# Kernel optimization log

Hardware: AMD Instinct MI355X
Metric: run time of the kernel (lower is better)

The kernel has to match this reference:

```python
import jax, jax.numpy as jnp
import numpy as np

B = 1024          # batch
H = 512           # hidden_dim
T = 256           # seq_len
CD = 2            # coord_dim
LAT = 64 + 64 + 128  # total latent dim


def setup_inputs() -> dict:
    key = jax.random.key(0)
    ks = jax.random.split(key, 20)
    s = 0.05  # weight init scale
    rn = lambda k, shp: (jax.random.normal(k, shp, dtype=jnp.float32) * s)
    return {
        "z_primitive": jax.random.normal(ks[0], (B, 64), dtype=jnp.float32),
        "z_skill": jax.random.normal(ks[1], (B, 64), dtype=jnp.float32),
        "z_style": jax.random.normal(ks[2], (B, 128), dtype=jnp.float32),
        "W_proj": rn(ks[3], (2 * H, LAT)),
        "b_proj": jnp.zeros((2 * H,), jnp.float32),
        "Wih1": rn(ks[4], (4 * H, CD)),
        "Whh1": rn(ks[5], (4 * H, H)),
        "bih1": jnp.zeros((4 * H,), jnp.float32),
        "bhh1": jnp.zeros((4 * H,), jnp.float32),
        "Wih2": rn(ks[6], (4 * H, H)),
        "Whh2": rn(ks[7], (4 * H, H)),
        "bih2": jnp.zeros((4 * H,), jnp.float32),
        "bhh2": jnp.zeros((4 * H,), jnp.float32),
        "Wo1": rn(ks[8], (H // 2, H)),
        "bo1": jnp.zeros((H // 2,), jnp.float32),
        "Wo2": rn(ks[9], (CD, H // 2)),
        "bo2": jnp.zeros((CD,), jnp.float32),
    }


def _lstm_cell(x, h, c, Wih, Whh, bih, bhh):
    # PyTorch gate order: i, f, g, o
    gates = x @ Wih.T + h @ Whh.T + (bih + bhh)
    i, f, g, o = jnp.split(gates, 4, axis=1)
    c_new = jax.nn.sigmoid(f) * c + jax.nn.sigmoid(i) * jnp.tanh(g)
    h_new = jax.nn.sigmoid(o) * jnp.tanh(c_new)
    return h_new, c_new


def reference(z_primitive, z_skill, z_style, W_proj, b_proj,
              Wih1, Whh1, bih1, bhh1, Wih2, Whh2, bih2, bhh2,
              Wo1, bo1, Wo2, bo2):
    z = jnp.concatenate([z_primitive, z_skill, z_style], axis=1)  # [B, LAT]
    init = z @ W_proj.T + b_proj                                  # [B, 2H]
    h0 = init[:, :H]
    c0 = init[:, H:]
    x0 = jnp.zeros((z.shape[0], CD), init.dtype)

    def step(carry, _):
        x, h1, c1, h2, c2 = carry
        h1, c1 = _lstm_cell(x, h1, c1, Wih1, Whh1, bih1, bhh1)
        h2, c2 = _lstm_cell(h1, h2, c2, Wih2, Whh2, bih2, bhh2)
        # output MLP (Dropout inactive in eval)
        y = jax.nn.relu(h2 @ Wo1.T + bo1) @ Wo2.T + bo2  # [B, CD]
        return (y, h1, c1, h2, c2), y

    # h0/c0 repeated across both LSTM layers (repeat(2,1,1) in torch)
    _, ys = jax.lax.scan(step, (x0, h0, c0, h0, c0), None, length=T)
    return jnp.transpose(ys, (1, 0, 2))  # [B, T, CD]
```

## Files before the change

kernel.cpp:

```cpp
#include <hip/hip_runtime.h>
#include <math.h>

#define NB 1024
#define NH 512
#define NT 256
#define NCD 2

typedef unsigned short u16;
typedef __bf16 bf16x8 __attribute__((ext_vector_type(8)));
typedef float  f32x4  __attribute__((ext_vector_type(4)));

#define MFMA_BF16 __builtin_amdgcn_mfma_f32_16x16x32_bf16

__device__ __forceinline__ float sigf(float x) { return 1.0f / (1.0f + expf(-x)); }
__device__ __forceinline__ float b2f(u16 u) {
    union { unsigned i; float f; } v; v.i = ((unsigned)u) << 16; return v.f;
}
__device__ __forceinline__ u16 f2b(float f) {
    union { float f; unsigned i; } v; v.f = f;
    unsigned r = v.i + 0x7fffu + ((v.i >> 16) & 1u);
    return (u16)(r >> 16);
}

__device__ __forceinline__ void async_cp16(const void* gptr, void* lptr) {
    __builtin_amdgcn_global_load_lds(
        (const __attribute__((address_space(1))) unsigned int*)gptr,
        (__attribute__((address_space(3))) unsigned int*)lptr,
        16, 0, 0);
}

__global__ __launch_bounds__(256) void convert3(
    const float* __restrict__ a, const float* __restrict__ b,
    const float* __restrict__ c,
    u16* __restrict__ oa, u16* __restrict__ ob, u16* __restrict__ oc)
{
    const int i = blockIdx.x * 256 + threadIdx.x;
    oa[i] = f2b(a[i]); ob[i] = f2b(b[i]); oc[i] = f2b(c[i]);
}

__global__ __launch_bounds__(256) void convw1(
    const float* __restrict__ a, u16* __restrict__ o)
{
    const int i = blockIdx.x * 256 + threadIdx.x;
    o[i] = f2b(a[i]);
}

__global__ __launch_bounds__(256) void bsum_k(
    const float* __restrict__ bi1, const float* __restrict__ bh1,
    const float* __restrict__ bi2, const float* __restrict__ bh2,
    float* __restrict__ o1, float* __restrict__ o2)
{
    const int i = blockIdx.x * 256 + threadIdx.x;
    o1[i] = bi1[i] + bh1[i];
    o2[i] = bi2[i] + bh2[i];
}

__global__ __launch_bounds__(256) void init_kernel(
    const float* __restrict__ zp, const float* __restrict__ zs,
    const float* __restrict__ zst, const float* __restrict__ Wp,
    const float* __restrict__ bp,
    u16* __restrict__ h1, float* __restrict__ c1,
    u16* __restrict__ h2, float* __restrict__ c2)
{
    __shared__ float z[4][256];
    const int tid = threadIdx.x;
    const int b0  = blockIdx.x * 4;
    for (int i = tid; i < 4 * 256; i += 256) {
        const int bb = i >> 8, k = i & 255;
        float v;
        if (k < 64)       v = zp [(b0 + bb) * 64  + k];
        else if (k < 128) v = zs [(b0 + bb) * 64  + (k - 64)];
        else              v = zst[(b0 + bb) * 128 + (k - 128)];
        z[bb][k] = v;
    }
    __syncthreads();
    for (int rt = 0; rt < 4; ++rt) {
        const int r = rt * 256 + tid;
        const float bias = bp[r];
        float a0 = bias, a1 = bias, a2 = bias, a3 = bias;
        for (int k = 0; k < 256; ++k) {
            const float w = Wp[r * 256 + k];
            a0 += z[0][k] * w; a1 += z[1][k] * w;
            a2 += z[2][k] * w; a3 += z[3][k] * w;
        }
        const float acc[4] = {a0, a1, a2, a3};
        for (int bb = 0; bb < 4; ++bb) {
            const int b = b0 + bb;
            if (r < NH) {
                h1[b * NH + r] = f2b(acc[bb]);
                h2[b * NH + r] = f2b(acc[bb]);
            } else {
                c1[b * NH + r - NH] = acc[bb];
                c2[b * NH + r - NH] = acc[bb];
            }
        }
    }
}

__global__ __launch_bounds__(512, 4) void fused_out_lstm1(
    const u16* __restrict__ h2prev,
    const u16* __restrict__ A0,
    const u16* __restrict__ W0,
    const float* __restrict__ bsum,
    const float* __restrict__ Wx,
    const u16* __restrict__ W1b,
    const float* __restrict__ bo1, const float* __restrict__ Wo2,
    const float* __restrict__ bo2, float* __restrict__ outp,
    float* __restrict__ c, u16* __restrict__ hnext,
    const int t, const int do_lstm)
{
    __shared__ __align__(16) char smem[61440];
    float* eg  = (float*)smem;
    float* red = (float*)(smem + 36864);

    const int tid  = threadIdx.x;
    const int lane = tid & 63;
    const int wv   = tid >> 6;
    const int g    = wv & 3;
    const int mh   = wv >> 2;
    const int l15  = lane & 15;
    const int q    = lane >> 4;
    const int bx   = blockIdx.x;
    const int ut   = (bx & 7) * 2 + ((bx >> 3) & 1);
    const int grp  = bx >> 4;
    const int b0   = grp * 32;
    const int u0   = ut * 32;

    int goffW0, goffW1, goffA = 0, goffO[4];
    {
        const int c0 = (wv * 2) * 64 + lane;
        const int w0r = c0 >> 3;
        goffW0 = ((w0r >> 5) * NH + u0 + (w0r & 31)) * NH + (((c0 & 7) ^ (w0r & 7)) * 8);
        const int c1i = (wv * 2 + 1) * 64 + lane;
        const int w1r = c1i >> 3;
        goffW1 = ((w1r >> 5) * NH + u0 + (w1r & 31)) * NH + (((c1i & 7) ^ (w1r & 7)) * 8);
        if (wv < 4) {
            const int ca = wv * 64 + lane;
            const int ar = ca >> 3;
            goffA = (b0 + ar) * NH + (((ca & 7) ^ (ar & 7)) * 8);
        }
#pragma unroll
        for (int i = 0; i < 4; ++i) {
            const int cidx = (wv * 4 + i) * 64 + lane;
            const int row  = cidx >> 3;
            const int kc   = (cidx & 7) ^ (row & 7);
            goffO[i] = row * NH + kc * 8;
        }
    }

    float r_x[4] = {0.f, 0.f, 0.f, 0.f};

    if (h2prev) {
        f32x4 acc_o[2][2];
#pragma unroll
        for (int mi = 0; mi < 2; ++mi)
#pragma unroll
            for (int ni = 0; ni < 2; ++ni)
                acc_o[mi][ni] = (f32x4){0.f, 0.f, 0.f, 0.f};

        for (int kk = 0; kk < 8; ++kk) {
            __syncthreads();
            const int k0 = kk * 64;
#pragma unroll
            for (int i = 0; i < 4; ++i)
                async_cp16((const void*)(W1b + goffO[i] + k0),
                           (void*)(smem + ((wv * 4 + i) << 10)));
            if (wv < 4)
                async_cp16((const void*)(h2prev + goffA + k0),
                           (void*)(smem + 32768 + (wv << 10)));
            asm volatile("s_waitcnt vmcnt(0)" ::: "memory");
            __builtin_amdgcn_s_barrier();
#pragma unroll
            for (int kh = 0; kh < 2; ++kh) {
                bf16x8 bfr[2], av[2];
#pragma unroll
                for (int ni = 0; ni < 2; ++ni) {
                    const int wrow = wv * 32 + ni * 16 + l15;
                    const int j = (kh * 4 + q) ^ (wrow & 7);
                    bfr[ni] = *(const bf16x8*)(smem + wrow * 128 + j * 16);
                }
#pragma unroll
                for (int mi = 0; mi < 2; ++mi) {
                    const int row = mi * 16 + l15;
                    const int j = (kh * 4 + q) ^ (row & 7);
                    av[mi] = *(const bf16x8*)(smem + 32768 + row * 128 + j * 16);
                }
#pragma unroll
                for (int mi = 0; mi < 2; ++mi)
#pragma unroll
                    for (int ni = 0; ni < 2; ++ni)
                        acc_o[mi][ni] = MFMA_BF16(av[mi], bfr[ni], acc_o[mi][ni], 0, 0, 0);
            }
        }
        float bo1n[2], w20[2], w21[2];
#pragma unroll
        for (int ni = 0; ni < 2; ++ni) {
            const int n = wv * 32 + ni * 16 + l15;
            bo1n[ni] = bo1[n]; w20[ni] = Wo2[n]; w21[ni] = Wo2[256 + n];
        }
        float pa[2][4], pb[2][4];
#pragma unroll
        for (int mi = 0; mi < 2; ++mi)
#pragma unroll
            for (int r = 0; r < 4; ++r) {
                const float s0 = fmaxf(acc_o[mi][0][r] + bo1n[0], 0.f);
                const float s1 = fmaxf(acc_o[mi][1][r] + bo1n[1], 0.f);
                pa[mi][r] = s0 * w20[0] + s1 * w20[1];
                pb[mi][r] = s0 * w21[0] + s1 * w21[1];
            }
#pragma unroll
        for (int off = 1; off < 16; off <<= 1)
#pragma unroll
            for (int mi = 0; mi < 2; ++mi)
#pragma unroll
                for (int r = 0; r < 4; ++r) {
                    pa[mi][r] += __shfl_xor(pa[mi][r], off, 64);
                    pb[mi][r] += __shfl_xor(pb[mi][r], off, 64);
                }
        if (l15 == 0) {
#pragma unroll
            for (int mi = 0; mi < 2; ++mi)
#pragma unroll
                for (int r = 0; r < 4; ++r) {
                    const int m = mi * 16 + q * 4 + r;
                    red[m * 16 + wv * 2 + 0] = pa[mi][r];
                    red[m * 16 + wv * 2 + 1] = pb[mi][r];
                }
        }
        __syncthreads();
        if (ut == 0 && tid < 64) {
            const int bl = tid >> 1, cc = tid & 1;
            float y = bo2[cc];
#pragma unroll
            for (int w8 = 0; w8 < 8; ++w8) y += red[bl * 16 + w8 * 2 + cc];
            outp[(size_t)(b0 + bl) * (NT * NCD) + (t - 1) * NCD + cc] = y;
        }
        if (do_lstm) {
            const int bq = tid >> 5;
#pragma unroll
            for (int jj = 0; jj < 2; ++jj)
#pragma unroll
                for (int cc = 0; cc < 2; ++cc) {
                    float y = bo2[cc];
#pragma unroll
                    for (int w8 = 0; w8 < 8; ++w8)
                        y += red[(bq * 2 + jj) * 16 + w8 * 2 + cc];
                    r_x[jj * 2 + cc] = y;
                }
        }
        __syncthreads();
    }
    if (!do_lstm) return;

    auto issue = [&](int m, int bi) {
        const int k0 = (m & 7) * 64;
        char* base = smem + bi * 20480;
        async_cp16((const void*)(W0 + goffW0 + k0),
                   (void*)(base + 4096 + (wv * 2) * 1024));
        async_cp16((const void*)(W0 + goffW1 + k0),
                   (void*)(base + 4096 + (wv * 2 + 1) * 1024));
        if (wv < 4)
            async_cp16((const void*)(A0 + goffA + k0),
                       (void*)(base + wv * 1024));
    };

    f32x4 acc[2];
    acc[0] = (f32x4){0.f, 0.f, 0.f, 0.f};
    acc[1] = (f32x4){0.f, 0.f, 0.f, 0.f};
    const int M = 8;
    issue(0, 0); issue(1, 1);
    int ci = 0;
    for (int m = 0; m < M; ++m) {
        if (m + 1 < M) {
            if (wv < 4) asm volatile("s_waitcnt vmcnt(3)" ::: "memory");
            else        asm volatile("s_waitcnt vmcnt(2)" ::: "memory");
        } else {
            asm volatile("s_waitcnt vmcnt(0)" ::: "memory");
        }
        __builtin_amdgcn_s_barrier();
        if (m + 2 < M) {
            int bi = ci + 2; if (bi >= 3) bi -= 3;
            issue(m + 2, bi);
        }
        const char* bA = smem + ci * 20480;
        const char* bW = bA + 4096;
#pragma unroll
        for (int khi = 0; khi < 2; ++khi) {
            bf16x8 bfr[2];
#pragma unroll
            for (int ni = 0; ni < 2; ++ni) {
                const int wrow = g * 32 + ni * 16 + l15;
                const int j = (khi * 4 + q) ^ (wrow & 7);
                bfr[ni] = *(const bf16x8*)(bW + wrow * 128 + j * 16);
            }
            const int row = mh * 16 + l15;
            const int j = (khi * 4 + q) ^ (row & 7);
            const bf16x8 av = *(const bf16x8*)(bA + row * 128 + j * 16);
            acc[0] = MFMA_BF16(av, bfr[0], acc[0], 0, 0, 0);
            acc[1] = MFMA_BF16(av, bfr[1], acc[1], 0, 0, 0);
        }
        ++ci; if (ci == 3) ci = 0;
    }

    __syncthreads();
#pragma unroll
    for (int ni = 0; ni < 2; ++ni)
#pragma unroll
        for (int r = 0; r < 4; ++r)
            eg[(g * 32 + mh * 16 + q * 4 + r) * 33 + ni * 16 + l15] = acc[ni][r];
    __syncthreads();

    const int u  = tid & 31;
    const int bq = tid >> 5;
    const int ug = u0 + u;
    float bs[4], wx0[4], wx1[4];
#pragma unroll
    for (int g4 = 0; g4 < 4; ++g4) bs[g4] = bsum[g4 * NH + ug];
#pragma unroll
    for (int g4 = 0; g4 < 4; ++g4) {
        wx0[g4] = Wx[(g4 * NH + ug) * 2 + 0];
        wx1[g4] = Wx[(g4 * NH + ug) * 2 + 1];
    }
#pragma unroll
    for (int jj = 0; jj < 2; ++jj) {
        const int bl = bq * 2 + jj;
        const int b  = b0 + bl;
        float gv[4];
#pragma unroll
        for (int g4 = 0; g4 < 4; ++g4) gv[g4] = eg[(g4 * 32 + bl) * 33 + u] + bs[g4];
        const float x0 = r_x[jj * 2 + 0];
        const float x1 = r_x[jj * 2 + 1];
#pragma unroll
        for (int g4 = 0; g4 < 4; ++g4) gv[g4] += x0 * wx0[g4] + x1 * wx1[g4];
        const float iv = sigf(gv[0]);
        const float fv = sigf(gv[1]);
        const float gg = tanhf(gv[2]);
        const float ov = sigf(gv[3]);
        const size_t idx = (size_t)b * NH + ug;
        const float cn = fv * c[idx] + iv * gg;
        c[idx] = cn;
        hnext[idx] = f2b(ov * tanhf(cn));
    }
}

__global__ __launch_bounds__(512, 4) void lstm_mfma32(
    const u16* __restrict__ A0, const u16* __restrict__ W0,
    const u16* __restrict__ A1, const u16* __restrict__ W1,
    const float* __restrict__ bsum,
    float* __restrict__ c, u16* __restrict__ hnext,
    const int npass)
{
    __shared__ __align__(16) char smem[61440];
    float* eg = (float*)smem;

    const int tid  = threadIdx.x;
    const int lane = tid & 63;
    const int wv   = tid >> 6;
    const int g    = wv & 3;
    const int mh   = wv >> 2;
    const int l15  = lane & 15;
    const int q    = lane >> 4;
    const int bx   = blockIdx.x;
    const int ut   = (bx & 7) * 2 + ((bx >> 3) & 1);
    const int grp  = bx >> 4;
    const int b0   = grp * 32;
    const int u0   = ut * 32;

    int goffW0, goffW1, goffA = 0;
    {
        const int c0 = (wv * 2) * 64 + lane;
        const int w0r = c0 >> 3;
        goffW0 = ((w0r >> 5) * NH + u0 + (w0r & 31)) * NH + (((c0 & 7) ^ (w0r & 7)) * 8);
        const int c1i = (wv * 2 + 1) * 64 + lane;
        const int w1r = c1i >> 3;
        goffW1 = ((w1r >> 5) * NH + u0 + (w1r & 31)) * NH + (((c1i & 7) ^ (w1r & 7)) * 8);
        if (wv < 4) {
            const int ca = wv * 64 + lane;
            const int ar = ca >> 3;
            goffA = (b0 + ar) * NH + (((ca & 7) ^ (ar & 7)) * 8);
        }
    }

    f32x4 acc[2];
    acc[0] = (f32x4){0.f, 0.f, 0.f, 0.f};
    acc[1] = (f32x4){0.f, 0.f, 0.f, 0.f};

    const int M = npass * 8;

    auto issue = [&](int m, int bi) {
        const u16* __restrict__ Ap = (m < 8) ? A0 : A1;
        const u16* __restrict__ Wp = (m < 8) ? W0 : W1;
        const int k0 = (m & 7) * 64;
        char* base = smem + bi * 20480;
        async_cp16((const void*)(Wp + goffW0 + k0),
                   (void*)(base + 4096 + (wv * 2) * 1024));
        async_cp16((const void*)(Wp + goffW1 + k0),
                   (void*)(base + 4096 + (wv * 2 + 1) * 1024));
        if (wv < 4)
            async_cp16((const void*)(Ap + goffA + k0),
                       (void*)(base + wv * 1024));
    };

    issue(0, 0);
    if (M > 1) issue(1, 1);
    int ci = 0;
    for (int m = 0; m < M; ++m) {
        if (m + 1 < M) {
            if (wv < 4) asm volatile("s_waitcnt vmcnt(3)" ::: "memory");
            else        asm volatile("s_waitcnt vmcnt(2)" ::: "memory");
        } else {
            asm volatile("s_waitcnt vmcnt(0)" ::: "memory");
        }
        __builtin_amdgcn_s_barrier();
        if (m + 2 < M) {
            int bi = ci + 2; if (bi >= 3) bi -= 3;
            issue(m + 2, bi);
        }
        const char* bA = smem + ci * 20480;
        const char* bW = bA + 4096;
#pragma unroll
        for (int khi = 0; khi < 2; ++khi) {
            bf16x8 bfr[2];
#pragma unroll
            for (int ni = 0; ni < 2; ++ni) {
                const int wrow = g * 32 + ni * 16 + l15;
                const int j = (khi * 4 + q) ^ (wrow & 7);
                bfr[ni] = *(const bf16x8*)(bW + wrow * 128 + j * 16);
            }
            const int row = mh * 16 + l15;
            const int j = (khi * 4 + q) ^ (row & 7);
            const bf16x8 av = *(const bf16x8*)(bA + row * 128 + j * 16);
            acc[0] = MFMA_BF16(av, bfr[0], acc[0], 0, 0, 0);
            acc[1] = MFMA_BF16(av, bfr[1], acc[1], 0, 0, 0);
        }
        ++ci; if (ci == 3) ci = 0;
    }

    __syncthreads();
#pragma unroll
    for (int ni = 0; ni < 2; ++ni)
#pragma unroll
        for (int r = 0; r < 4; ++r)
            eg[(g * 32 + mh * 16 + q * 4 + r) * 33 + ni * 16 + l15] = acc[ni][r];
    __syncthreads();

    const int u  = tid & 31;
    const int bq = tid >> 5;
    const int ug = u0 + u;
    float bs[4];
#pragma unroll
    for (int g4 = 0; g4 < 4; ++g4) bs[g4] = bsum[g4 * NH + ug];
#pragma unroll
    for (int jj = 0; jj < 2; ++jj) {
        const int bl = bq * 2 + jj;
        const int b  = b0 + bl;
        float gv[4];
#pragma unroll
        for (int g4 = 0; g4 < 4; ++g4) gv[g4] = eg[(g4 * 32 + bl) * 33 + u] + bs[g4];
        const float iv = sigf(gv[0]);
        const float fv = sigf(gv[1]);
        const float gg = tanhf(gv[2]);
        const float ov = sigf(gv[3]);
        const size_t idx = (size_t)b * NH + ug;
        const float cn = fv * c[idx] + iv * gg;
        c[idx] = cn;
        hnext[idx] = f2b(ov * tanhf(cn));
    }
}

extern "C" void kernel_launch(void* const* d_in, const int* in_sizes, int n_in,
                              void* d_out, int out_size, void* d_ws, size_t ws_size,
                              hipStream_t stream)
{
    const float* zp   = (const float*)d_in[0];
    const float* zsk  = (const float*)d_in[1];
    const float* zst  = (const float*)d_in[2];
    const float* Wp   = (const float*)d_in[3];
    const float* bp   = (const float*)d_in[4];
    const float* Wih1 = (const float*)d_in[5];
    const float* Whh1 = (const float*)d_in[6];
    const float* bih1 = (const float*)d_in[7];
    const float* bhh1 = (const float*)d_in[8];
    const float* Wih2 = (const float*)d_in[9];
    const float* Whh2 = (const float*)d_in[10];
    const float* bih2 = (const float*)d_in[11];
    const float* bhh2 = (const float*)d_in[12];
    const float* Wo1  = (const float*)d_in[13];
    const float* bo1  = (const float*)d_in[14];
    const float* Wo2  = (const float*)d_in[15];
    const float* bo2  = (const float*)d_in[16];

    const size_t BH = (size_t)NB * NH;
    u16*   h1a   = (u16*)d_ws;
    u16*   h1b   = h1a + BH;
    u16*   h2a   = h1b + BH;
    u16*   h2b   = h2a + BH;
    float* c1    = (float*)(h2b + BH);
    float* c2    = c1 + BH;
    float* bs1   = c2 + BH;
    float* bs2   = bs1 + 2048;
    u16*   Wo1b  = (u16*)(bs2 + 2048);
    u16*   Whh1b = Wo1b + 131072;
    u16*   Wih2b = Whh1b + 1048576;
    u16*   Whh2b = Wih2b + 1048576;

    convert3<<<(2048 * 512) / 256, 256, 0, stream>>>(Whh1, Wih2, Whh2, Whh1b, Wih2b, Whh2b);
    convw1<<<(256 * 512) / 256, 256, 0, stream>>>(Wo1, Wo1b);
    bsum_k<<<2048 / 256, 256, 0, stream>>>(bih1, bhh1, bih2, bhh2, bs1, bs2);
    init_kernel<<<NB / 4, 256, 0, stream>>>(zp, zsk, zst, Wp, bp, h1a, c1, h2a, c2);

    u16* h1c = h1a; u16* h1n = h1b;
    u16* h2c = h2a; u16* h2n = h2b;
    float* outp = (float*)d_out;
    for (int t = 0; t < NT; ++t) {
        fused_out_lstm1<<<512, 512, 0, stream>>>(
            (t == 0) ? (const u16*)0 : h2c, h1c, Whh1b, bs1, Wih1,
            Wo1b, bo1, Wo2, bo2, outp, c1, h1n, t, 1);
        lstm_mfma32<<<512, 512, 0, stream>>>(h1n, Wih2b, h2c, Whh2b,
                                             bs2, c2, h2n, 2);
        u16* tmp = h1c; h1c = h1n; h1n = tmp;
        tmp = h2c; h2c = h2n; h2n = tmp;
    }
    fused_out_lstm1<<<512, 512, 0, stream>>>(
        h2c, h1c, Whh1b, bs1, Wih1,
        Wo1b, bo1, Wo2, bo2, outp, c1, h1n, NT, 0);
}
```

Baseline: 7.518 ms.

## Triple-buffer output-MLP GEMM loads with async prefetch two k-steps ahead

Replaces the synchronous 8-step, 64-wide k loop of the output projection with a 16-step, 32-wide k loop over three rotating LDS buffers. Async copies for steps k+1 and k+2 stay in flight while step k computes, using partial vmcnt waits instead of draining all loads each iteration. The swizzle is changed to a 4-chunk pattern and the reduction scratch is moved to a higher offset so it does not overlap the new buffers. The aim is to hide global load latency in this per-timestep kernel. The cost is more LDS use, more barriers per tile, and vmcnt counts that depend on exactly how many copies each wave issues.

After: 8.183 ms. 1.09x slower.

```diff
diff --git a/kernel.cpp b/kernel.cpp
--- a/kernel.cpp
+++ b/kernel.cpp
@@ -111,7 +111,7 @@
 {
     __shared__ __align__(16) char smem[61440];
     float* eg  = (float*)smem;
-    float* red = (float*)(smem + 36864);
+    float* red = (float*)(smem + 55296);
 
     const int tid  = threadIdx.x;
     const int lane = tid & 63;
@@ -126,7 +126,7 @@
     const int b0   = grp * 32;
     const int u0   = ut * 32;
 
-    int goffW0, goffW1, goffA = 0, goffO[4];
+    int goffW0, goffW1, goffA = 0;
     {
         const int c0 = (wv * 2) * 64 + lane;
         const int w0r = c0 >> 3;
@@ -139,13 +139,20 @@
             const int ar = ca >> 3;
             goffA = (b0 + ar) * NH + (((ca & 7) ^ (ar & 7)) * 8);
         }
-#pragma unroll
-        for (int i = 0; i < 4; ++i) {
-            const int cidx = (wv * 4 + i) * 64 + lane;
-            const int row  = cidx >> 3;
-            const int kc   = (cidx & 7) ^ (row & 7);
-            goffO[i] = row * NH + kc * 8;
-        }
+    }
+    int goffO[2], goffA2 = 0;
+#pragma unroll
+    for (int i = 0; i < 2; ++i) {
+        const int cidx = (wv * 2 + i) * 64 + lane;
+        const int row  = cidx >> 2;
+        const int j    = cidx & 3;
+        goffO[i] = row * NH + ((j ^ (row & 3)) * 8);
+    }
+    if (wv < 2) {
+        const int ca  = wv * 64 + lane;
+        const int row = ca >> 2;
+        const int j   = ca & 3;
+        goffA2 = (b0 + row) * NH + ((j ^ (row & 3)) * 8);
     }
 
     float r_x[4] = {0.f, 0.f, 0.f, 0.f};
@@ -158,40 +165,55 @@
             for (int ni = 0; ni < 2; ++ni)
                 acc_o[mi][ni] = (f32x4){0.f, 0.f, 0.f, 0.f};
 
-        for (int kk = 0; kk < 8; ++kk) {
-            __syncthreads();
-            const int k0 = kk * 64;
-#pragma unroll
-            for (int i = 0; i < 4; ++i)
-                async_cp16((const void*)(W1b + goffO[i] + k0),
-                           (void*)(smem + ((wv * 4 + i) << 10)));
-            if (wv < 4)
-                async_cp16((const void*)(h2prev + goffA + k0),
-                           (void*)(smem + 32768 + (wv << 10)));
-            asm volatile("s_waitcnt vmcnt(0)" ::: "memory");
+        auto issueA = [&](int kk, int bi) {
+            const int k0 = kk * 32;
+            char* base = smem + bi * 18432;
+            async_cp16((const void*)(W1b + goffO[0] + k0),
+                       (void*)(base + (wv * 2) * 1024));
+            async_cp16((const void*)(W1b + goffO[1] + k0),
+                       (void*)(base + (wv * 2 + 1) * 1024));
+            if (wv < 2)
+                async_cp16((const void*)(h2prev + goffA2 + k0),
+                           (void*)(base + 16384 + (wv << 10)));
+        };
+
+        issueA(0, 0); issueA(1, 1);
+        int ai = 0;
+        for (int kk = 0; kk < 16; ++kk) {
+            if (kk + 1 < 16) {
+                if (wv < 2) asm volatile("s_waitcnt vmcnt(3)" ::: "memory");
+                else        asm volatile("s_waitcnt vmcnt(2)" ::: "memory");
+            } else {
+                asm volatile("s_waitcnt vmcnt(0)" ::: "memory");
+            }
             __builtin_amdgcn_s_barrier();
-#pragma unroll
-            for (int kh = 0; kh < 2; ++kh) {
-                bf16x8 bfr[2], av[2];
-#pragma unroll
-                for (int ni = 0; ni < 2; ++ni) {
-                    const int wrow = wv * 32 + ni * 16 + l15;
-                    const int j = (kh * 4 + q) ^ (wrow & 7);
-                    bfr[ni] = *(const bf16x8*)(smem + wrow * 128 + j * 16);
-                }
-#pragma unroll
-                for (int mi = 0; mi < 2; ++mi) {
-                    const int row = mi * 16 + l15;
-                    const int j = (kh * 4 + q) ^ (row & 7);
-                    av[mi] = *(const bf16x8*)(smem + 32768 + row * 128 + j * 16);
-                }
-#pragma unroll
-                for (int mi = 0; mi < 2; ++mi)
-#pragma unroll
-                    for (int ni = 0; ni < 2; ++ni)
-                        acc_o[mi][ni] = MFMA_BF16(av[mi], bfr[ni], acc_o[mi][ni], 0, 0, 0);
-            }
-        }
+            if (kk + 2 < 16) {
+                int bi = ai + 2; if (bi >= 3) bi -= 3;
+                issueA(kk + 2, bi);
+            }
+            const char* bB  = smem + ai * 18432;
+            const char* bA2 = bB + 16384;
+            bf16x8 bfr[2], av[2];
+#pragma unroll
+            for (int ni = 0; ni < 2; ++ni) {
+                const int wrow = wv * 32 + ni * 16 + l15;
+                const int j = q ^ (wrow & 3);
+                bfr[ni] = *(const bf16x8*)(bB + wrow * 64 + j * 16);
+            }
+#pragma unroll
+            for (int mi = 0; mi < 2; ++mi) {
+                const int row = mi * 16 + l15;
+                const int j = q ^ (row & 3);
+                av[mi] = *(const bf16x8*)(bA2 + row * 64 + j * 16);
+            }
+#pragma unroll
+            for (int mi = 0; mi < 2; ++mi)
+#pragma unroll
+                for (int ni = 0; ni < 2; ++ni)
+                    acc_o[mi][ni] = MFMA_BF16(av[mi], bfr[ni], acc_o[mi][ni], 0, 0, 0);
+            ++ai; if (ai == 3) ai = 0;
+        }
+
         float bo1n[2], w20[2], w21[2];
 #pragma unroll
         for (int ni = 0; ni < 2; ++ni) {
```
